# Performance work log

Hardware: AMD Instinct MI355X
Metric: run time of the kernel (lower is better)

The kernel has to match this reference:

```python
import jax, jax.numpy as jnp
import numpy as np

B, S, D, E, H = 4, 2048, 1024, 8, 4096

def setup_inputs() -> dict:
    key = jax.random.key(0)
    ks = jax.random.split(key, 7)
    scale_d = 1.0 / np.sqrt(D)
    scale_h = 1.0 / np.sqrt(H)
    return {
        "x": jax.random.normal(ks[0], (B, S, D), dtype=jnp.float32),
        "Wr": jax.random.uniform(ks[1], (D, E), jnp.float32, -scale_d, scale_d),
        "br": jnp.zeros((E,), jnp.float32),
        "W1": jax.random.uniform(ks[2], (E, D, H), jnp.float32, -scale_d, scale_d),
        "b1": jax.random.uniform(ks[3], (E, H), jnp.float32, -scale_d, scale_d),
        "W2": jax.random.uniform(ks[4], (E, H, D), jnp.float32, -scale_h, scale_h),
        "b2": jax.random.uniform(ks[5], (E, D), jnp.float32, -scale_h, scale_h),
    }

def reference(x, Wr, br, W1, b1, W2, b2):
    # Router: softmax then argmax (top-1). Note: original does NOT scale
    # expert output by the routing weight and never applies capacity drop.
    route_logits = jnp.einsum("bsd,de->bse", x, Wr) + br
    routing_weights = jax.nn.softmax(route_logits, axis=-1)
    selected_expert = jnp.argmax(routing_weights, axis=-1)  # [B, S] int

    num_experts = W1.shape[0]
    out = jnp.zeros_like(x)
    # Fixed small loop over experts (structurally distinct weight slices);
    # select-by-mask keeps shapes static under jit.
    for e in range(num_experts):
        h = jax.nn.gelu(jnp.einsum("bsd,dh->bsh", x, W1[e]) + b1[e], approximate=False)
        y = jnp.einsum("bsh,hd->bsd", h, W2[e]) + b2[e]
        out = jnp.where((selected_expert == e)[..., None], y, out)
    return out
```

## Files before the change

### kernel.cpp

```cpp
#include <hip/hip_runtime.h>
#include <math.h>

#define TOK   8192
#define DD    1024
#define EE    8
#define HH    4096
#define MAXROWS 9216
#define MAXMT 72

typedef unsigned short u16;
typedef unsigned int   u32;
typedef __bf16 bf16x8 __attribute__((ext_vector_type(8)));
typedef float  f32x16 __attribute__((ext_vector_type(16)));

__device__ __forceinline__ u16 f2bf(float f) {
  union { float f; u32 u; } v; v.f = f;
  u32 r = v.u + 0x7fffu + ((v.u >> 16) & 1u);
  return (u16)(r >> 16);
}

__device__ __forceinline__ void gload16(const void* g, void* l) {
  __builtin_amdgcn_global_load_lds(
      (const __attribute__((address_space(1))) void*)g,
      (__attribute__((address_space(3))) void*)l, 16, 0, 0);
}

__global__ void k_init(int* rowmap, int* counts, int* fill) {
  int i = blockIdx.x * 256 + threadIdx.x;
  if (i < MAXROWS) rowmap[i] = -1;
  if (blockIdx.x == 0 && threadIdx.x < EE) { counts[threadIdx.x] = 0; fill[threadIdx.x] = 0; }
}

__global__ __launch_bounds__(256)
void k_route(const float* __restrict__ x, const float* __restrict__ Wr,
             const float* __restrict__ br, int* __restrict__ eid,
             int* __restrict__ counts, u16* __restrict__ xb) {
  int t = blockIdx.x * 4 + (threadIdx.x >> 6);
  int lt = threadIdx.x & 63;
  const float4* xr = (const float4*)(x + (size_t)t * DD);
  u16* xbr = xb + (size_t)t * DD;
  const float4* wrp = (const float4*)Wr;
  float acc[EE];
  #pragma unroll
  for (int e = 0; e < EE; ++e) acc[e] = 0.f;
  #pragma unroll
  for (int i = 0; i < 4; ++i) {
    int d4 = lt + 64 * i;
    float4 v = xr[d4];
    u32 p0 = (u32)f2bf(v.x) | ((u32)f2bf(v.y) << 16);
    u32 p1 = (u32)f2bf(v.z) | ((u32)f2bf(v.w) << 16);
    ((uint2*)xbr)[d4] = make_uint2(p0, p1);
    float vv[4] = { v.x, v.y, v.z, v.w };
    #pragma unroll
    for (int dd = 0; dd < 4; ++dd) {
      float xv = vv[dd];
      float4 a = wrp[(size_t)(d4 * 4 + dd) * 2];
      float4 b = wrp[(size_t)(d4 * 4 + dd) * 2 + 1];
      acc[0] += xv * a.x; acc[1] += xv * a.y; acc[2] += xv * a.z; acc[3] += xv * a.w;
      acc[4] += xv * b.x; acc[5] += xv * b.y; acc[6] += xv * b.z; acc[7] += xv * b.w;
    }
  }
  #pragma unroll
  for (int e = 0; e < EE; ++e)
    #pragma unroll
    for (int off = 32; off > 0; off >>= 1) acc[e] += __shfl_down(acc[e], off);
  if (lt == 0) {
    float best = -1e30f; int be = 0;
    #pragma unroll
    for (int e = 0; e < EE; ++e) {
      float v = acc[e] + br[e];
      if (v > best) { best = v; be = e; }
    }
    eid[t] = be;
    atomicAdd(&counts[be], 1);
  }
}

__global__ void k_scan(const int* __restrict__ counts, int* __restrict__ poff) {
  if (threadIdx.x == 0) {
    int off = 0; poff[0] = 0;
    for (int e = 0; e < EE; ++e) { off += ((counts[e] + 127) >> 7) << 7; poff[e + 1] = off; }
  }
}

__global__ void k_fillmap(const int* __restrict__ eid, const int* __restrict__ poff,
                          int* __restrict__ fill, int* __restrict__ rowmap) {
  int t = blockIdx.x * 256 + threadIdx.x;
  if (t < TOK) {
    int e = eid[t];
    int pos = atomicAdd(&fill[e], 1);
    rowmap[poff[e] + pos] = t;
  }
}

__global__ __launch_bounds__(256)
void k_transpose(const float* __restrict__ W, u16* __restrict__ WT, int K, int N) {
  __shared__ float tile[32][33];
  int e = blockIdx.z;
  int n0 = blockIdx.x * 32, k0 = blockIdx.y * 32;
  const float* We = W + (size_t)e * K * N;
  u16* WTe = WT + (size_t)e * K * N;
  int tx = threadIdx.x & 31, ty = threadIdx.x >> 5;
  #pragma unroll
  for (int i = 0; i < 4; ++i)
    tile[ty + 8 * i][tx] = We[(size_t)(k0 + ty + 8 * i) * N + n0 + tx];
  __syncthreads();
  #pragma unroll
  for (int i = 0; i < 4; ++i)
    WTe[(size_t)(n0 + ty + 8 * i) * K + k0 + tx] = f2bf(tile[tx][ty + 8 * i]);
}

template <int KDIM, int NDIM, bool G2>
__global__ __launch_bounds__(256, 3)
void k_gemm(const u16* __restrict__ Abase, const u16* __restrict__ WT,
            const float* __restrict__ bias, const int* __restrict__ poff,
            const int* __restrict__ rowmap, u16* __restrict__ hout,
            float* __restrict__ yout) {
  const int mt = blockIdx.y;
  const int mbase = mt * 128;
  if (mbase >= poff[EE]) return;
  int e = 0;
  #pragma unroll
  for (int q = 1; q < EE; ++q) e += (mbase >= poff[q]) ? 1 : 0;

  const int nbase = blockIdx.x * 128;
  const int tid = threadIdx.x;
  const int w = tid >> 6;
  const int lt = tid & 63;
  const int wr = w >> 1, wc = w & 1;

  __shared__ u16 lsA[2][128 * 32];
  __shared__ u16 lsB[2][128 * 32];

  const int srow = lt >> 2;
  const int clog = (lt & 3) ^ (srow & 3);
  int ar0, ar1;
  if (G2) { ar0 = mbase + w * 16 + srow; ar1 = ar0 + 64; }
  else {
    ar0 = rowmap[mbase + w * 16 + srow];      if (ar0 < 0) ar0 = 0;
    ar1 = rowmap[mbase + 64 + w * 16 + srow]; if (ar1 < 0) ar1 = 0;
  }
  const u16* gA0 = Abase + (size_t)ar0 * KDIM + clog * 8;
  const u16* gA1 = Abase + (size_t)ar1 * KDIM + clog * 8;
  const u16* wte = WT + (size_t)e * NDIM * KDIM + (size_t)nbase * KDIM;
  const u16* gB0 = wte + (size_t)(w * 16 + srow) * KDIM + clog * 8;
  const u16* gB1 = wte + (size_t)(64 + w * 16 + srow) * KDIM + clog * 8;

  f32x16 acc[2][2] = {};

  #define STAGE(buf, koff)                                          \
    do {                                                            \
      gload16(gA0 + (koff), &lsA[buf][(w * 16) * 32]);              \
      gload16(gA1 + (koff), &lsA[buf][(64 + w * 16) * 32]);         \
      gload16(gB0 + (koff), &lsB[buf][(w * 16) * 32]);              \
      gload16(gB1 + (koff), &lsB[buf][(64 + w * 16) * 32]);         \
    } while (0)

  STAGE(0, 0);
  const int KT = KDIM / 32;
  for (int bk = 0; bk < KT; ++bk) {
    __syncthreads();
    if (bk + 1 < KT) STAGE((bk + 1) & 1, (bk + 1) * 32);
    const u16* A = lsA[bk & 1];
    const u16* B = lsB[bk & 1];
    #pragma unroll
    for (int s = 0; s < 2; ++s) {
      bf16x8 af[2], bg[2];
      #pragma unroll
      for (int i = 0; i < 2; ++i) {
        int row = wr * 64 + i * 32 + (lt & 31);
        int phys = (s * 2 + (lt >> 5)) ^ (row & 3);
        af[i] = *(const bf16x8*)&A[row * 32 + phys * 8];
      }
      #pragma unroll
      for (int j = 0; j < 2; ++j) {
        int nn = wc * 64 + j * 32 + (lt & 31);
        int phys = (s * 2 + (lt >> 5)) ^ (nn & 3);
        bg[j] = *(const bf16x8*)&B[nn * 32 + phys * 8];
      }
      #pragma unroll
      for (int i = 0; i < 2; ++i)
        #pragma unroll
        for (int j = 0; j < 2; ++j)
          acc[i][j] = __builtin_amdgcn_mfma_f32_32x32x16_bf16(af[i], bg[j], acc[i][j], 0, 0, 0);
    }
  }
  #undef STAGE

  float bv[2];
  #pragma unroll
  for (int j = 0; j < 2; ++j)
    bv[j] = bias[(size_t)e * NDIM + nbase + wc * 64 + j * 32 + (lt & 31)];

  #pragma unroll
  for (int i = 0; i < 2; ++i) {
    const int rbase = wr * 64 + i * 32 + 4 * (lt >> 5);
    #pragma unroll
    for (int r = 0; r < 16; ++r) {
      const int rl = rbase + (r & 3) + 8 * (r >> 2);
      const int grow = mbase + rl;
      if (G2) {
        int tok = rowmap[grow];
        if (tok >= 0) {
          float* yp = yout + (size_t)tok * NDIM + nbase + wc * 64 + (lt & 31);
          #pragma unroll
          for (int j = 0; j < 2; ++j) yp[j * 32] = acc[i][j][r] + bv[j];
        }
      } else {
        u16* hp = hout + (size_t)grow * NDIM + nbase + wc * 64 + (lt & 31);
        #pragma unroll
        for (int j = 0; j < 2; ++j) {
          float v = acc[i][j][r] + bv[j];
          v = 0.5f * v * (1.0f + erff(v * 0.70710678118654752f));
          hp[j * 32] = f2bf(v);
        }
      }
    }
  }
}

extern "C" void kernel_launch(void* const* d_in, const int* in_sizes, int n_in,
                              void* d_out, int out_size, void* d_ws, size_t ws_size,
                              hipStream_t stream) {
  const float* x  = (const float*)d_in[0];
  const float* Wr = (const float*)d_in[1];
  const float* br = (const float*)d_in[2];
  const float* W1 = (const float*)d_in[3];
  const float* b1 = (const float*)d_in[4];
  const float* W2 = (const float*)d_in[5];
  const float* b2 = (const float*)d_in[6];
  float* out = (float*)d_out;

  char* ws = (char*)d_ws;
  int* eid    = (int*)(ws + 0);
  int* counts = (int*)(ws + 32768);
  int* fill   = (int*)(ws + 32768 + 64);
  int* poff   = (int*)(ws + 32768 + 128);
  int* rowmap = (int*)(ws + 33024);
  u16* xbf    = (u16*)(ws + 69888);
  u16* w1t    = (u16*)(ws + 16847104);
  u16* w2t    = (u16*)(ws + 83955968);
  u16* hbuf   = (u16*)(ws + 151064832);

  k_init<<<MAXROWS / 256, 256, 0, stream>>>(rowmap, counts, fill);
  k_route<<<TOK / 4, 256, 0, stream>>>(x, Wr, br, eid, counts, xbf);
  k_scan<<<1, 64, 0, stream>>>(counts, poff);
  k_fillmap<<<TOK / 256, 256, 0, stream>>>(eid, poff, fill, rowmap);
  k_transpose<<<dim3(HH / 32, DD / 32, EE), 256, 0, stream>>>(W1, w1t, DD, HH);
  k_transpose<<<dim3(DD / 32, HH / 32, EE), 256, 0, stream>>>(W2, w2t, HH, DD);
  k_gemm<DD, HH, false><<<dim3(HH / 128, MAXMT), 256, 0, stream>>>(xbf, w1t, b1, poff, rowmap, hbuf, nullptr);
  k_gemm<HH, DD, true><<<dim3(DD / 128, MAXMT), 256, 0, stream>>>(hbuf, w2t, b2, poff, rowmap, nullptr, out);
}
```

Before: 723.5 us.

## Triple-buffer GEMM loads, split-K second GEMM, widen transpose tiles

The weight transpose now uses 64x64 tiles with float4 loads and ushort4 stores. The GEMM becomes a three-stage LDS pipeline with explicit vmcnt waits and one barrier per K step, and the shared-memory layout drops the XOR swizzle. The second GEMM is split along K into two partial buffers (reusing the W1 transpose region), and a new reduce kernel adds the partials and the bias. This aims to hide global load latency and to fill more CUs in the K=4096 GEMM, at the cost of extra partial-buffer traffic and one more launch.

```diff
diff --git a/kernel.cpp b/kernel.cpp
--- a/kernel.cpp
+++ b/kernel.cpp
@@ -95,88 +95,100 @@
 
 __global__ __launch_bounds__(256)
 void k_transpose(const float* __restrict__ W, u16* __restrict__ WT, int K, int N) {
-  __shared__ float tile[32][33];
+  __shared__ float tile[64][65];
   int e = blockIdx.z;
-  int n0 = blockIdx.x * 32, k0 = blockIdx.y * 32;
+  int n0 = blockIdx.x * 64, k0 = blockIdx.y * 64;
   const float* We = W + (size_t)e * K * N;
   u16* WTe = WT + (size_t)e * K * N;
-  int tx = threadIdx.x & 31, ty = threadIdx.x >> 5;
-  #pragma unroll
-  for (int i = 0; i < 4; ++i)
-    tile[ty + 8 * i][tx] = We[(size_t)(k0 + ty + 8 * i) * N + n0 + tx];
+  int tx = threadIdx.x & 15, ty = threadIdx.x >> 4;
+  #pragma unroll
+  for (int i = 0; i < 4; ++i) {
+    int r = ty + 16 * i;
+    float4 v = *(const float4*)&We[(size_t)(k0 + r) * N + n0 + tx * 4];
+    tile[r][tx * 4 + 0] = v.x; tile[r][tx * 4 + 1] = v.y;
+    tile[r][tx * 4 + 2] = v.z; tile[r][tx * 4 + 3] = v.w;
+  }
   __syncthreads();
   #pragma unroll
-  for (int i = 0; i < 4; ++i)
-    WTe[(size_t)(n0 + ty + 8 * i) * K + k0 + tx] = f2bf(tile[tx][ty + 8 * i]);
-}
-
-template <int KDIM, int NDIM, bool G2>
+  for (int i = 0; i < 4; ++i) {
+    int n = ty + 16 * i;
+    ushort4 o;
+    o.x = f2bf(tile[tx * 4 + 0][n]); o.y = f2bf(tile[tx * 4 + 1][n]);
+    o.z = f2bf(tile[tx * 4 + 2][n]); o.w = f2bf(tile[tx * 4 + 3][n]);
+    *(ushort4*)&WTe[(size_t)(n0 + n) * K + k0 + tx * 4] = o;
+  }
+}
+
+template <int KDIM, int NDIM, bool G2, int KSPLIT>
 __global__ __launch_bounds__(256, 3)
 void k_gemm(const u16* __restrict__ Abase, const u16* __restrict__ WT,
             const float* __restrict__ bias, const int* __restrict__ poff,
             const int* __restrict__ rowmap, u16* __restrict__ hout,
             float* __restrict__ yout) {
-  const int mt = blockIdx.y;
-  const int mbase = mt * 128;
+  const int mbase = blockIdx.y * 128;
   if (mbase >= poff[EE]) return;
   int e = 0;
   #pragma unroll
   for (int q = 1; q < EE; ++q) e += (mbase >= poff[q]) ? 1 : 0;
-
   const int nbase = blockIdx.x * 128;
+  const int koff = blockIdx.z * (KDIM / KSPLIT);
+  constexpr int KT = KDIM / (32 * KSPLIT);
+
   const int tid = threadIdx.x;
-  const int w = tid >> 6;
-  const int lt = tid & 63;
+  const int w = tid >> 6, lt = tid & 63;
   const int wr = w >> 1, wc = w & 1;
 
-  __shared__ u16 lsA[2][128 * 32];
-  __shared__ u16 lsB[2][128 * 32];
-
-  const int srow = lt >> 2;
-  const int clog = (lt & 3) ^ (srow & 3);
-  int ar0, ar1;
-  if (G2) { ar0 = mbase + w * 16 + srow; ar1 = ar0 + 64; }
+  __shared__ u16 ls[3][2][4096];
+
+  const int rl0 = (w * 4 + 0 + (lt >> 5)) * 8 + (lt & 7);
+  const int rl1 = (w * 4 + 2 + (lt >> 5)) * 8 + (lt & 7);
+  const int ck = (lt >> 3) & 3;
+  int arow0, arow1;
+  if (G2) { arow0 = mbase + rl0; arow1 = mbase + rl1; }
   else {
-    ar0 = rowmap[mbase + w * 16 + srow];      if (ar0 < 0) ar0 = 0;
-    ar1 = rowmap[mbase + 64 + w * 16 + srow]; if (ar1 < 0) ar1 = 0;
-  }
-  const u16* gA0 = Abase + (size_t)ar0 * KDIM + clog * 8;
-  const u16* gA1 = Abase + (size_t)ar1 * KDIM + clog * 8;
-  const u16* wte = WT + (size_t)e * NDIM * KDIM + (size_t)nbase * KDIM;
-  const u16* gB0 = wte + (size_t)(w * 16 + srow) * KDIM + clog * 8;
-  const u16* gB1 = wte + (size_t)(64 + w * 16 + srow) * KDIM + clog * 8;
+    arow0 = rowmap[mbase + rl0]; if (arow0 < 0) arow0 = 0;
+    arow1 = rowmap[mbase + rl1]; if (arow1 < 0) arow1 = 0;
+  }
+  const u16* gA0 = Abase + (size_t)arow0 * KDIM + koff + ck * 8;
+  const u16* gA1 = Abase + (size_t)arow1 * KDIM + koff + ck * 8;
+  const u16* wte = WT + (size_t)e * NDIM * KDIM + koff;
+  const u16* gB0 = wte + (size_t)(nbase + rl0) * KDIM + ck * 8;
+  const u16* gB1 = wte + (size_t)(nbase + rl1) * KDIM + ck * 8;
+
+  #define STAGE(bi, ko)                                   \
+    do {                                                  \
+      gload16(gA0 + (ko), &ls[bi][0][(w * 128) * 8]);     \
+      gload16(gA1 + (ko), &ls[bi][0][(w * 128 + 64) * 8]);\
+      gload16(gB0 + (ko), &ls[bi][1][(w * 128) * 8]);     \
+      gload16(gB1 + (ko), &ls[bi][1][(w * 128 + 64) * 8]);\
+    } while (0)
 
   f32x16 acc[2][2] = {};
-
-  #define STAGE(buf, koff)                                          \
-    do {                                                            \
-      gload16(gA0 + (koff), &lsA[buf][(w * 16) * 32]);              \
-      gload16(gA1 + (koff), &lsA[buf][(64 + w * 16) * 32]);         \
-      gload16(gB0 + (koff), &lsB[buf][(w * 16) * 32]);              \
-      gload16(gB1 + (koff), &lsB[buf][(64 + w * 16) * 32]);         \
-    } while (0)
-
   STAGE(0, 0);
-  const int KT = KDIM / 32;
+  STAGE(1, 32);
+
+  int sbuf = 2, cbuf = 0;
   for (int bk = 0; bk < KT; ++bk) {
-    __syncthreads();
-    if (bk + 1 < KT) STAGE((bk + 1) & 1, (bk + 1) * 32);
-    const u16* A = lsA[bk & 1];
-    const u16* B = lsB[bk & 1];
+    if (bk + 1 < KT) asm volatile("s_waitcnt vmcnt(4) lgkmcnt(0)\ns_barrier" ::: "memory");
+    else             asm volatile("s_waitcnt vmcnt(0) lgkmcnt(0)\ns_barrier" ::: "memory");
+    if (bk + 2 < KT) STAGE(sbuf, (bk + 2) * 32);
+    const u16* A = ls[cbuf][0];
+    const u16* B = ls[cbuf][1];
     #pragma unroll
     for (int s = 0; s < 2; ++s) {
+      const int cc = s * 2 + (lt >> 5);
       bf16x8 af[2], bg[2];
       #pragma unroll
       for (int i = 0; i < 2; ++i) {
-        int row = wr * 64 + i * 32 + (lt & 31);
-        int phys = (s * 2 + (lt >> 5)) ^ (row & 3);
-        af[i] = *(const bf16x8*)&A[row * 32 + phys * 8];
+        int r = wr * 64 + i * 32 + (lt & 31);
+        int slot = ((r >> 3) << 5) + cc * 8 + (r & 7);
+        af[i] = *(const bf16x8*)&A[slot * 8];
       }
       #pragma unroll
       for (int j = 0; j < 2; ++j) {
-        int nn = wc * 64 + j * 32 + (lt & 31);
-        int phys = (s * 2 + (lt >> 5)) ^ (nn & 3);
-        bg[j] = *(const bf16x8*)&B[nn * 32 + phys * 8];
+        int n = wc * 64 + j * 32 + (lt & 31);
+        int slot = ((n >> 3) << 5) + cc * 8 + (n & 7);
+        bg[j] = *(const bf16x8*)&B[slot * 8];
       }
       #pragma unroll
       for (int i = 0; i < 2; ++i)
@@ -184,30 +196,39 @@
         for (int j = 0; j < 2; ++j)
           acc[i][j] = __builtin_amdgcn_mfma_f32_32x32x16_bf16(af[i], bg[j], acc[i][j], 0, 0, 0);
     }
+    cbuf = (cbuf == 2) ? 0 : cbuf + 1;
+    sbuf = (sbuf == 2) ? 0 : sbuf + 1;
   }
   #undef STAGE
 
-  float bv[2];
-  #pragma unroll
-  for (int j = 0; j < 2; ++j)
-    bv[j] = bias[(size_t)e * NDIM + nbase + wc * 64 + j * 32 + (lt & 31)];
-
-  #pragma unroll
-  for (int i = 0; i < 2; ++i) {
-    const int rbase = wr * 64 + i * 32 + 4 * (lt >> 5);
-    #pragma unroll
-    for (int r = 0; r < 16; ++r) {
-      const int rl = rbase + (r & 3) + 8 * (r >> 2);
-      const int grow = mbase + rl;
-      if (G2) {
-        int tok = rowmap[grow];
+  if (G2) {
+    float* yo = yout + (size_t)blockIdx.z * ((size_t)TOK * DD);
+    #pragma unroll
+    for (int i = 0; i < 2; ++i) {
+      const int rbase = wr * 64 + i * 32 + 4 * (lt >> 5);
+      #pragma unroll
+      for (int r = 0; r < 16; ++r) {
+        const int rl = rbase + (r & 3) + 8 * (r >> 2);
+        int tok = rowmap[mbase + rl];
         if (tok >= 0) {
-          float* yp = yout + (size_t)tok * NDIM + nbase + wc * 64 + (lt & 31);
+          float* yp = yo + (size_t)tok * NDIM + nbase + wc * 64 + (lt & 31);
           #pragma unroll
-          for (int j = 0; j < 2; ++j) yp[j * 32] = acc[i][j][r] + bv[j];
+          for (int j = 0; j < 2; ++j) yp[j * 32] = acc[i][j][r];
         }
-      } else {
-        u16* hp = hout + (size_t)grow * NDIM + nbase + wc * 64 + (lt & 31);
+      }
+    }
+  } else {
+    float bv[2];
+    #pragma unroll
+    for (int j = 0; j < 2; ++j)
+      bv[j] = bias[(size_t)e * NDIM + nbase + wc * 64 + j * 32 + (lt & 31)];
+    #pragma unroll
+    for (int i = 0; i < 2; ++i) {
+      const int rbase = wr * 64 + i * 32 + 4 * (lt >> 5);
+      #pragma unroll
+      for (int r = 0; r < 16; ++r) {
+        const int rl = rbase + (r & 3) + 8 * (r >> 2);
+        u16* hp = hout + (size_t)(mbase + rl) * NDIM + nbase + wc * 64 + (lt & 31);
         #pragma unroll
         for (int j = 0; j < 2; ++j) {
           float v = acc[i][j][r] + bv[j];
@@ -217,6 +238,20 @@
       }
     }
   }
+}
+
+__global__ void k_reduce(const float* __restrict__ p0, const float* __restrict__ p1,
+                         const float* __restrict__ b2, const int* __restrict__ eid,
+                         float* __restrict__ out) {
+  int i = blockIdx.x * 256 + threadIdx.x;
+  int tok = i >> 8;
+  int d4 = i & 255;
+  int e = eid[tok];
+  float4 b = ((const float4*)(b2 + (size_t)e * DD))[d4];
+  float4 a0 = ((const float4*)p0)[i];
+  float4 a1 = ((const float4*)p1)[i];
+  ((float4*)out)[i] = make_float4(b.x + a0.x + a1.x, b.y + a0.y + a1.y,
+                                  b.z + a0.z + a1.z, b.w + a0.w + a1.w);
 }
 
 extern "C" void kernel_launch(void* const* d_in, const int* in_sizes, int n_in,
@@ -241,13 +276,15 @@
   u16* w1t    = (u16*)(ws + 16847104);
   u16* w2t    = (u16*)(ws + 83955968);
   u16* hbuf   = (u16*)(ws + 151064832);
+  float* pbuf = (float*)w1t;
 
   k_init<<<MAXROWS / 256, 256, 0, stream>>>(rowmap, counts, fill);
   k_route<<<TOK / 4, 256, 0, stream>>>(x, Wr, br, eid, counts, xbf);
   k_scan<<<1, 64, 0, stream>>>(counts, poff);
   k_fillmap<<<TOK / 256, 256, 0, stream>>>(eid, poff, fill, rowmap);
-  k_transpose<<<dim3(HH / 32, DD / 32, EE), 256, 0, stream>>>(W1, w1t, DD, HH);
-  k_transpose<<<dim3(DD / 32, HH / 32, EE), 256, 0, stream>>>(W2, w2t, HH, DD);
-  k_gemm<DD, HH, false><<<dim3(HH / 128, MAXMT), 256, 0, stream>>>(xbf, w1t, b1, poff, rowmap, hbuf, nullptr);
-  k_gemm<HH, DD, true><<<dim3(DD / 128, MAXMT), 256, 0, stream>>>(hbuf, w2t, b2, poff, rowmap, nullptr, out);
-}
+  k_transpose<<<dim3(HH / 64, DD / 64, EE), 256, 0, stream>>>(W1, w1t, DD, HH);
+  k_transpose<<<dim3(DD / 64, HH / 64, EE), 256, 0, stream>>>(W2, w2t, HH, DD);
+  k_gemm<DD, HH, false, 1><<<dim3(HH / 128, MAXMT, 1), 256, 0, stream>>>(xbf, w1t, b1, poff, rowmap, hbuf, nullptr);
+  k_gemm<HH, DD, true, 2><<<dim3(DD / 128, MAXMT, 2), 256, 0, stream>>>(hbuf, w2t, nullptr, poff, rowmap, nullptr, pbuf);
+  k_reduce<<<TOK * DD / 1024, 256, 0, stream>>>(pbuf, pbuf + (size_t)TOK * DD, b2, eid, out);
+}
```

After: 793.5 us. +9.7%, slower.
